# Optimization experiments

Hardware: AMD Instinct MI355X
Metric: run time of the kernel (lower is better)

The kernel has to match this reference:

```python
import jax, jax.numpy as jnp
import numpy as np

B, N = 32, 1024
STEPS = 6

def setup_inputs() -> dict:
    key = jax.random.key(0)
    ks = jax.random.split(key, 20)
    # index columns: residue (<20), element (<5), ordinal position (<21)
    res = jax.random.randint(ks[0], (B, N, 1), 0, 20)
    atom = jax.random.randint(ks[1], (B, N, 1), 0, 5)
    cnt = jax.random.randint(ks[2], (B, N, 1), 0, 21)
    x_int = jnp.concatenate([res, atom, cnt], axis=2)
    x_xyz = jax.random.normal(ks[3], (B, N, 3), dtype=jnp.float32)
    def lin(k, out_d, in_d):
        s = 1.0 / np.sqrt(in_d)
        kw, kb = jax.random.split(k)
        return (jax.random.uniform(kw, (out_d, in_d), jnp.float32, -s, s),
                jax.random.uniform(kb, (out_d,), jnp.float32, -s, s))
    xyz_w, xyz_b = lin(ks[4], 172, 3)
    up_w, up_b = lin(ks[5], 1024, 256)
    att1_w, att1_b = lin(ks[6], 128, 2048)
    att2_w, att2_b = lin(ks[7], 1, 128)
    energy_w, energy_b = lin(ks[8], 1, 1024)
    s = 1.0 / np.sqrt(1024)
    w_ih = jax.random.uniform(ks[9], (4096, 2048), jnp.float32, -s, s)
    w_hh = jax.random.uniform(ks[10], (4096, 1024), jnp.float32, -s, s)
    b_ih = jax.random.uniform(ks[11], (4096,), jnp.float32, -s, s)
    b_hh = jax.random.uniform(ks[12], (4096,), jnp.float32, -s, s)
    amino_embed = jax.random.normal(ks[13], (20, 28), dtype=jnp.float32)
    element_embed = jax.random.normal(ks[14], (5, 28), dtype=jnp.float32)
    position_embed = jax.random.normal(ks[15], (21, 28), dtype=jnp.float32)
    return dict(x_int=x_int, x_xyz=x_xyz,
                amino_embed=amino_embed, element_embed=element_embed,
                position_embed=position_embed, xyz_w=xyz_w, xyz_b=xyz_b,
                up_w=up_w, up_b=up_b, w_ih=w_ih, w_hh=w_hh, b_ih=b_ih, b_hh=b_hh,
                att1_w=att1_w, att1_b=att1_b, att2_w=att2_w, att2_b=att2_b,
                energy_w=energy_w, energy_b=energy_b)

def reference(x_int, x_xyz, amino_embed, element_embed, position_embed,
              xyz_w, xyz_b, up_w, up_b, w_ih, w_hh, b_ih, b_hh,
              att1_w, att1_b, att2_w, att2_b, energy_w, energy_b):
    # embed_atoms: [B,N,28]*3 + [B,N,172] -> [B,N,256]
    emb = jnp.concatenate([
        amino_embed[x_int[:, :, 0]],
        element_embed[x_int[:, :, 1]],
        position_embed[x_int[:, :, 2]],
        jax.nn.relu(jnp.einsum('bnd,od->bno', x_xyz, xyz_w) + xyz_b),
    ], axis=2)
    x = jnp.einsum('bnd,od->bno', emb, up_w) + up_b  # [B,N,1024]
    b = x.shape[0]
    h = jnp.zeros((b, 1024), x.dtype)
    c = jnp.zeros((b, 1024), x.dtype)
    input_embed = jnp.concatenate([x.mean(axis=1), jnp.zeros((b, 1024), x.dtype)], axis=1)
    for _ in range(STEPS):
        # single LSTM cell step (seq_len=1); PyTorch gate order i,f,g,o
        gates = input_embed @ w_ih.T + b_ih + h @ w_hh.T + b_hh
        ig, fg, gg, og = jnp.split(gates, 4, axis=1)
        c = jax.nn.sigmoid(fg) * c + jax.nn.sigmoid(ig) * jnp.tanh(gg)
        h = jax.nn.sigmoid(og) * jnp.tanh(c)
        read = h  # [B,1024]
        # attention MLP over the concat [read | x]: split the 2048-dim GEMM
        a1 = jax.nn.relu(jnp.einsum('bnd,od->bno', x, att1_w[:, 1024:])
                         + (read @ att1_w[:, :1024].T)[:, None, :] + att1_b)
        logits = jnp.einsum('bnk,ok->bno', a1, att2_w) + att2_b  # [B,N,1]
        w = jax.nn.softmax(logits, axis=1)
        pooled = (w * x).sum(axis=1)  # [B,1024]
        input_embed = jnp.concatenate([pooled, read], axis=1)
    return c @ energy_w.T + energy_b  # [B,1]
```

## Files before the change

### kernel.cpp

```cpp
#include <hip/hip_runtime.h>
#include <math.h>

#define BB 32
#define NN 1024
#define BN (BB*NN)
#define KS 24
#define KCH 128

__device__ __forceinline__ float sigmoidf_(float v) { return 1.0f / (1.0f + expf(-v)); }
__device__ __forceinline__ unsigned f2bf(float f) {
  unsigned u = __float_as_uint(f);
  return (u + 0x7fffu + ((u >> 16) & 1u)) >> 16;
}

__global__ void k_zero(float* __restrict__ h, float* __restrict__ c) {
  int i = blockIdx.x * 256 + threadIdx.x;
  h[i] = 0.0f; c[i] = 0.0f;
}

__global__ void k_emb(const int* __restrict__ xint, const float* __restrict__ xyz,
                      const float* __restrict__ am, const float* __restrict__ el,
                      const float* __restrict__ po, const float* __restrict__ xw,
                      const float* __restrict__ xb, float* __restrict__ emb,
                      unsigned* __restrict__ embh) {
  __shared__ float sv[256];
  int row = blockIdx.x;
  int d = threadIdx.x;
  int i0 = xint[row*3+0], i1 = xint[row*3+1], i2 = xint[row*3+2];
  float v;
  if (d < 28)        v = am[i0*28 + d];
  else if (d < 56)   v = el[i1*28 + (d-28)];
  else if (d < 84)   v = po[i2*28 + (d-56)];
  else {
    int o = d - 84;
    float x0 = xyz[row*3+0], x1 = xyz[row*3+1], x2 = xyz[row*3+2];
    v = fmaxf(xw[o*3+0]*x0 + xw[o*3+1]*x1 + xw[o*3+2]*x2 + xb[o], 0.0f);
  }
  emb[(size_t)row*256 + d] = v;
  sv[d] = v;
  __syncthreads();
  if (d < 128) {
    unsigned u = (f2bf(sv[d*2+1]) << 16) | f2bf(sv[d*2]);
    embh[(size_t)row*128 + d] = u;
  }
}

__global__ __launch_bounds__(256) void k_wt(const float* __restrict__ w_ih,
        const float* __restrict__ w_hh, unsigned* __restrict__ wt2) {
  __shared__ float t[32][33];
  int jt = blockIdx.x * 32, kt = blockIdx.y * 32;
  int tx = threadIdx.x & 31, ty = threadIdx.x >> 5;
#pragma unroll
  for (int i = 0; i < 4; i++) {
    int j = jt + ty + i*8;
    int k = kt + tx;
    float v = (k < 2048) ? w_ih[(size_t)j*2048 + k] : w_hh[(size_t)j*1024 + (k - 2048)];
    t[ty + i*8][tx] = v;
  }
  __syncthreads();
#pragma unroll
  for (int i = 0; i < 2; i++) {
    int kl2 = ty + i*8;
    float lo = t[tx][kl2*2], hi = t[tx][kl2*2+1];
    unsigned u = (f2bf(hi) << 16) | f2bf(lo);
    wt2[(size_t)((kt >> 1) + kl2)*4096 + jt + tx] = u;
  }
}

__global__ void k_wc1(const float* __restrict__ up_w, const float* __restrict__ att1w,
                      float* __restrict__ wcp) {
  int k = blockIdx.x;
  int och = blockIdx.y;
  int d = threadIdx.x;
  __shared__ float s[128];
  int o0 = och*128;
  if (d < 128) s[d] = att1w[(size_t)k*2048 + 1024 + o0 + d];
  __syncthreads();
  float acc = 0.0f;
#pragma unroll 8
  for (int oi = 0; oi < 128; oi++) acc += up_w[(size_t)(o0+oi)*256 + d] * s[oi];
  wcp[((size_t)och*128 + k)*256 + d] = acc;
}

__global__ void k_wc2(const float* __restrict__ wcp, float* __restrict__ wc) {
  int k = blockIdx.x, d = threadIdx.x;
  float s = 0.0f;
#pragma unroll
  for (int p = 0; p < 8; p++) s += wcp[((size_t)p*128 + k)*256 + d];
  wc[k*256 + d] = s;
}

__global__ void k_bc(const float* __restrict__ up_b, const float* __restrict__ att1w,
                     float* __restrict__ bc) {
  int k = blockIdx.x;
  int t = threadIdx.x;
  float acc = 0.0f;
#pragma unroll
  for (int i = 0; i < 4; i++) {
    int o = i*256 + t*4;
    float4 a4 = *(const float4*)(att1w + (size_t)k*2048 + 1024 + o);
    float4 b4 = *(const float4*)(up_b + o);
    acc += a4.x*b4.x + a4.y*b4.y + a4.z*b4.z + a4.w*b4.w;
  }
#pragma unroll
  for (int m = 32; m >= 1; m >>= 1) acc += __shfl_xor(acc, m, 64);
  if (t == 0) bc[k] = acc;
}

__global__ __launch_bounds__(256) void k_gemm32(const float* __restrict__ A,
        const float* __restrict__ W, const float* __restrict__ bias,
        float* __restrict__ C) {
  __shared__ float As[32][33];
  __shared__ float Bs[32][132];
  const int m0 = blockIdx.x * 32;
  const int tid = threadIdx.x;
  const int tx = tid & 15, ty = tid >> 4;
  float acc[2][8];
#pragma unroll
  for (int i = 0; i < 2; i++)
#pragma unroll
    for (int j = 0; j < 8; j++) acc[i][j] = 0.0f;

  for (int kt = 0; kt < 256; kt += 32) {
    {
      int r = tid >> 3;
      int kq = (tid & 7) * 4;
      float4 a4 = *(const float4*)(A + (size_t)(m0 + r)*256 + kt + kq);
      As[kq+0][r] = a4.x; As[kq+1][r] = a4.y; As[kq+2][r] = a4.z; As[kq+3][r] = a4.w;
    }
#pragma unroll
    for (int i = 0; i < 4; i++) {
      int s = tid + i*256;
      int n = s >> 3;
      int kq = (s & 7) * 4;
      float4 b4 = *(const float4*)(W + (size_t)n*256 + kt + kq);
      Bs[kq+0][n] = b4.x; Bs[kq+1][n] = b4.y; Bs[kq+2][n] = b4.z; Bs[kq+3][n] = b4.w;
    }
    __syncthreads();
#pragma unroll
    for (int kk = 0; kk < 32; kk++) {
      float a0 = As[kk][ty*2], a1 = As[kk][ty*2+1];
      float4 b0 = *(const float4*)&Bs[kk][tx*4];
      float4 b1 = *(const float4*)&Bs[kk][64 + tx*4];
      float bv[8] = {b0.x,b0.y,b0.z,b0.w,b1.x,b1.y,b1.z,b1.w};
#pragma unroll
      for (int j = 0; j < 8; j++) { acc[0][j] += a0*bv[j]; acc[1][j] += a1*bv[j]; }
    }
    __syncthreads();
  }
#pragma unroll
  for (int i = 0; i < 2; i++) {
    int row = m0 + ty*2 + i;
#pragma unroll
    for (int ch = 0; ch < 2; ch++) {
      int col = ch*64 + tx*4;
      float4 o;
      o.x = acc[i][ch*4+0] + bias[col+0];
      o.y = acc[i][ch*4+1] + bias[col+1];
      o.z = acc[i][ch*4+2] + bias[col+2];
      o.w = acc[i][ch*4+3] + bias[col+3];
      *(float4*)(C + (size_t)row*128 + col) = o;
    }
  }
}

__global__ __launch_bounds__(256) void k_gates(const float* __restrict__ P, const float* __restrict__ h,
        const unsigned* __restrict__ wt2, float* __restrict__ gp) {
  __shared__ float Xs[32][KCH];
  int jb = blockIdx.x;
  int ks = blockIdx.y;
  int tid = threadIdx.x;
  int kglob = ks * KCH;
  const float* src; int soff;
  if (ks < 8)       { src = P; soff = kglob; }
  else if (ks < 16) { src = h; soff = kglob - 1024; }
  else              { src = h; soff = kglob - 2048; }
#pragma unroll
  for (int i = 0; i < 4; i++) {
    int s = tid + i*256;
    int b = s >> 5, k4 = s & 31;
    *(float4*)&Xs[b][k4*4] = *(const float4*)(src + b*1024 + soff + k4*4);
  }
  __syncthreads();

  int jg = tid & 31, bg = tid >> 5;
  int j0 = jb*128 + jg*4;
  int b0 = bg*4;
  const unsigned* wr = wt2 + (size_t)(ks*64)*4096 + j0;
  float acc[4][4];
#pragma unroll
  for (int i = 0; i < 4; i++)
#pragma unroll
    for (int j = 0; j < 4; j++) acc[i][j] = 0.0f;

  for (int k2 = 0; k2 < KCH/2; k2++) {
    uint4 u4 = *(const uint4*)(wr + (size_t)k2*4096);
    float wlo[4], whi[4];
    wlo[0] = __uint_as_float(u4.x << 16); whi[0] = __uint_as_float(u4.x & 0xffff0000u);
    wlo[1] = __uint_as_float(u4.y << 16); whi[1] = __uint_as_float(u4.y & 0xffff0000u);
    wlo[2] = __uint_as_float(u4.z << 16); whi[2] = __uint_as_float(u4.z & 0xffff0000u);
    wlo[3] = __uint_as_float(u4.w << 16); whi[3] = __uint_as_float(u4.w & 0xffff0000u);
    int k = k2*2;
#pragma unroll
    for (int bi = 0; bi < 4; bi++) {
      float x0 = Xs[b0+bi][k], x1 = Xs[b0+bi][k+1];
#pragma unroll
      for (int ji = 0; ji < 4; ji++) acc[ji][bi] += wlo[ji]*x0 + whi[ji]*x1;
    }
  }
#pragma unroll
  for (int bi = 0; bi < 4; bi++) {
    float4 v = make_float4(acc[0][bi], acc[1][bi], acc[2][bi], acc[3][bi]);
    *(float4*)(gp + ((size_t)ks*32 + b0 + bi)*4096 + j0) = v;
  }
}

__global__ __launch_bounds__(256) void k_lstm_rap(const float* __restrict__ gp,
        const float* __restrict__ b_ih, const float* __restrict__ b_hh,
        float* __restrict__ c, float* __restrict__ h,
        const float* __restrict__ att1w, float* __restrict__ rap, int need_ra) {
  int wb = blockIdx.x;
  int b = wb >> 2, dch = wb & 3;
  int tid = threadIdx.x;
  int d = dch*256 + tid;
  __shared__ float hs[256];
  float gi = b_ih[d]        + b_hh[d];
  float gf = b_ih[1024 + d] + b_hh[1024 + d];
  float gg = b_ih[2048 + d] + b_hh[2048 + d];
  float go = b_ih[3072 + d] + b_hh[3072 + d];
#pragma unroll 4
  for (int ks = 0; ks < KS; ks++) {
    const float* base = gp + ((size_t)ks*32 + b)*4096;
    gi += base[d]; gf += base[1024 + d]; gg += base[2048 + d]; go += base[3072 + d];
  }
  size_t ci = (size_t)b*1024 + d;
  float cn = sigmoidf_(gf)*c[ci] + sigmoidf_(gi)*tanhf(gg);
  c[ci] = cn;
  float hn = sigmoidf_(go)*tanhf(cn);
  h[ci] = hn;
  hs[tid] = hn;
  __syncthreads();
  if (need_ra) {
    int k = tid >> 1, half = tid & 1;
    const float* wr = att1w + (size_t)k*2048 + dch*256 + half*128;
    float acc = 0.0f;
#pragma unroll 8
    for (int i = 0; i < 32; i++) {
      float4 w4 = *(const float4*)(wr + i*4);
      int dl = half*128 + i*4;
      acc += w4.x*hs[dl] + w4.y*hs[dl+1] + w4.z*hs[dl+2] + w4.w*hs[dl+3];
    }
    acc += __shfl_xor(acc, 1, 64);
    if (half == 0) rap[((size_t)dch*32 + b)*128 + k] = acc;
  }
}

__global__ __launch_bounds__(256) void k_logits(const float* __restrict__ xa,
        const float* __restrict__ rap, const float* __restrict__ att1b,
        const float* __restrict__ att2w, const float* __restrict__ att2b,
        float* __restrict__ lg) {
  int b = blockIdx.x, nc = blockIdx.y;
  int t = threadIdx.x;
  __shared__ float rb[128], w2[128];
  if (t < 128) {
    float r = rap[(size_t)(0  + b)*128 + t] + rap[(size_t)(32 + b)*128 + t]
            + rap[(size_t)(64 + b)*128 + t] + rap[(size_t)(96 + b)*128 + t];
    rb[t] = r + att1b[t];
    w2[t] = att2w[t];
  }
  __syncthreads();
  int n = nc*128 + (t >> 1);
  int half = (t & 1) * 64;
  const float* xr = xa + ((size_t)b*1024 + n)*128 + half;
  float acc = 0.0f;
#pragma unroll
  for (int i = 0; i < 16; i++) {
    int kk = i*4;
    float4 v = *(const float4*)(xr + kk);
    int kg = half + kk;
    acc += fmaxf(v.x + rb[kg+0], 0.0f)*w2[kg+0]
         + fmaxf(v.y + rb[kg+1], 0.0f)*w2[kg+1]
         + fmaxf(v.z + rb[kg+2], 0.0f)*w2[kg+2]
         + fmaxf(v.w + rb[kg+3], 0.0f)*w2[kg+3];
  }
  acc += __shfl_xor(acc, 1, 64);
  if ((t & 1) == 0) lg[(size_t)b*1024 + n] = acc + att2b[0];
}

__global__ __launch_bounds__(256) void k_poolemb(const unsigned* __restrict__ embh,
        const float* __restrict__ lg, float* __restrict__ pp) {
  int wb = blockIdx.x;
  int b = wb >> 2, nch = wb & 3;
  int tid = threadIdx.x;
  __shared__ float ws[256];
  __shared__ float red[256];
  if (lg) {
    float mx = -1e30f;
#pragma unroll
    for (int i = 0; i < 4; i++) mx = fmaxf(mx, lg[b*1024 + tid + i*256]);
    red[tid] = mx; __syncthreads();
    for (int s = 128; s > 0; s >>= 1) { if (tid < s) red[tid] = fmaxf(red[tid], red[tid+s]); __syncthreads(); }
    float m = red[0]; __syncthreads();
    float sum = 0.0f;
#pragma unroll
    for (int i = 0; i < 4; i++) sum += expf(lg[b*1024 + tid + i*256] - m);
    red[tid] = sum; __syncthreads();
    for (int s = 128; s > 0; s >>= 1) { if (tid < s) red[tid] += red[tid+s]; __syncthreads(); }
    float inv = 1.0f / red[0];
    __syncthreads();
    ws[tid] = expf(lg[b*1024 + nch*256 + tid] - m) * inv;
  } else {
    ws[tid] = 1.0f;
  }
  __syncthreads();
  int pu = tid & 127, ng = tid >> 7;
  const unsigned* eb = embh + (size_t)(b*1024 + nch*256 + ng*128)*128 + pu;
  float a0 = 0.0f, a1 = 0.0f;
#pragma unroll 4
  for (int n = 0; n < 128; n++) {
    unsigned u = eb[(size_t)n*128];
    float w = ws[ng*128 + n];
    a0 += w * __uint_as_float(u << 16);
    a1 += w * __uint_as_float(u & 0xffff0000u);
  }
  int p = nch*2 + ng;
  pp[((size_t)p*32 + b)*256 + pu*2]     = a0;
  pp[((size_t)p*32 + b)*256 + pu*2 + 1] = a1;
}

__global__ __launch_bounds__(256) void k_pool_pgemm(const float* __restrict__ pp,
        const float* __restrict__ up_w, const float* __restrict__ up_b,
        float* __restrict__ Pout, float scale) {
  int wb = blockIdx.x;
  int b = wb >> 2, oc = wb & 3;
  int tid = threadIdx.x;
  __shared__ float pe[256];
  float s = 0.0f;
#pragma unroll
  for (int p = 0; p < 8; p++) s += pp[((size_t)p*32 + b)*256 + tid];
  pe[tid] = s * scale;
  __syncthreads();
  int o = oc*256 + tid;
  const float* wr = up_w + (size_t)o*256;
  float acc = up_b[o];
#pragma unroll 8
  for (int d = 0; d < 256; d += 4) {
    float4 w4 = *(const float4*)(wr + d);
    acc += w4.x*pe[d] + w4.y*pe[d+1] + w4.z*pe[d+2] + w4.w*pe[d+3];
  }
  Pout[(size_t)b*1024 + o] = acc;
}

__global__ void k_out(const float* __restrict__ c, const float* __restrict__ ew,
                      const float* __restrict__ eb, float* __restrict__ out) {
  int b = blockIdx.x, t = threadIdx.x;
  float acc = 0.0f;
  for (int d = t; d < 1024; d += 64) acc += c[b*1024 + d] * ew[d];
  for (int off = 32; off > 0; off >>= 1) acc += __shfl_down(acc, off, 64);
  if (t == 0) out[b] = acc + eb[0];
}

extern "C" void kernel_launch(void* const* d_in, const int* in_sizes, int n_in,
                              void* d_out, int out_size, void* d_ws, size_t ws_size,
                              hipStream_t stream) {
  const int*   x_int  = (const int*)d_in[0];
  const float* x_xyz  = (const float*)d_in[1];
  const float* am     = (const float*)d_in[2];
  const float* el     = (const float*)d_in[3];
  const float* po     = (const float*)d_in[4];
  const float* xyz_w  = (const float*)d_in[5];
  const float* xyz_b  = (const float*)d_in[6];
  const float* up_w   = (const float*)d_in[7];
  const float* up_b   = (const float*)d_in[8];
  const float* w_ih   = (const float*)d_in[9];
  const float* w_hh   = (const float*)d_in[10];
  const float* b_ih   = (const float*)d_in[11];
  const float* b_hh   = (const float*)d_in[12];
  const float* att1_w = (const float*)d_in[13];
  const float* att1_b = (const float*)d_in[14];
  const float* att2_w = (const float*)d_in[15];
  const float* att2_b = (const float*)d_in[16];
  const float* en_w   = (const float*)d_in[17];
  const float* en_b   = (const float*)d_in[18];
  float* out = (float*)d_out;

  char* ws = (char*)d_ws;
  size_t off = 0;
  auto alloc = [&](size_t bytes) { void* p = ws + off; off += (bytes + 255) & ~(size_t)255; return p; };
  float*    emb  = (float*)alloc((size_t)BN*256*4);
  unsigned* embh = (unsigned*)alloc((size_t)BN*128*4);
  unsigned* wt2  = (unsigned*)alloc((size_t)1536*4096*4);
  float*    xa   = (float*)alloc((size_t)BN*128*4);
  float*    wcp  = (float*)alloc((size_t)8*128*256*4);
  float*    wc   = (float*)alloc((size_t)128*256*4);
  float*    bc   = (float*)alloc((size_t)128*4);
  float*    gp   = (float*)alloc((size_t)KS*32*4096*4);
  float*    pp   = (float*)alloc((size_t)8*32*256*4);
  float*    P    = (float*)alloc((size_t)32*1024*4);
  float*    h    = (float*)alloc((size_t)32*1024*4);
  float*    c    = (float*)alloc((size_t)32*1024*4);
  float*    rap  = (float*)alloc((size_t)4*32*128*4);
  float*    lg   = (float*)alloc((size_t)32*1024*4);
  (void)ws_size; (void)in_sizes; (void)n_in; (void)out_size;

  k_zero<<<128, 256, 0, stream>>>(h, c);
  k_emb<<<BN, 256, 0, stream>>>(x_int, x_xyz, am, el, po, xyz_w, xyz_b, emb, embh);
  k_wt<<<dim3(128, 96), 256, 0, stream>>>(w_ih, w_hh, wt2);
  k_wc1<<<dim3(128, 8), 256, 0, stream>>>(up_w, att1_w, wcp);
  k_wc2<<<128, 256, 0, stream>>>(wcp, wc);
  k_bc<<<128, 64, 0, stream>>>(up_b, att1_w, bc);
  k_gemm32<<<BN/32, 256, 0, stream>>>(emb, wc, bc, xa);
  k_poolemb<<<128, 256, 0, stream>>>(embh, nullptr, pp);
  k_pool_pgemm<<<128, 256, 0, stream>>>(pp, up_w, up_b, P, 1.0f/1024.0f);

  for (int step = 0; step < 6; step++) {
    k_gates<<<dim3(32, KS), 256, 0, stream>>>(P, h, wt2, gp);
    k_lstm_rap<<<128, 256, 0, stream>>>(gp, b_ih, b_hh, c, h, att1_w, rap, step < 5 ? 1 : 0);
    if (step < 5) {
      k_logits<<<dim3(32, 8), 256, 0, stream>>>(xa, rap, att1_b, att2_w, att2_b, lg);
      k_poolemb<<<128, 256, 0, stream>>>(embh, lg, pp);
      k_pool_pgemm<<<128, 256, 0, stream>>>(pp, up_w, up_b, P, 1.0f);
    }
  }
  k_out<<<32, 64, 0, stream>>>(c, en_w, en_b, out);
}
```

Baseline: 434.6 us.

## Fuse attention logits into pooling, store projected x in bf16, skip zero-h gates

Merges the logits kernel into the pooling kernel, so each block recomputes the logits for its whole batch row into shared memory instead of reading them from a global buffer. This removes a launch and a round trip through global memory on every step. The precomputed attention projection xa is now stored as bf16, halving the bytes read each step at some cost in precision. The first LSTM step launches only the input-part K-slices, because h starts at zero, so h no longer needs zeroing. The trade-off is redundancy: each of the 4 blocks per batch now recomputes all 1024 logits, which is 4x the logit arithmetic and xa reads.

```diff
diff --git a/kernel.cpp b/kernel.cpp
--- a/kernel.cpp
+++ b/kernel.cpp
@@ -12,10 +12,12 @@
   unsigned u = __float_as_uint(f);
   return (u + 0x7fffu + ((u >> 16) & 1u)) >> 16;
 }
-
-__global__ void k_zero(float* __restrict__ h, float* __restrict__ c) {
+__device__ __forceinline__ float bflo(unsigned u) { return __uint_as_float(u << 16); }
+__device__ __forceinline__ float bfhi(unsigned u) { return __uint_as_float(u & 0xffff0000u); }
+
+__global__ void k_zero(float* __restrict__ c) {
   int i = blockIdx.x * 256 + threadIdx.x;
-  h[i] = 0.0f; c[i] = 0.0f;
+  c[i] = 0.0f;
 }
 
 __global__ void k_emb(const int* __restrict__ xint, const float* __restrict__ xyz,
@@ -109,9 +111,9 @@
 
 __global__ __launch_bounds__(256) void k_gemm32(const float* __restrict__ A,
         const float* __restrict__ W, const float* __restrict__ bias,
-        float* __restrict__ C) {
+        unsigned* __restrict__ Ch) {
   __shared__ float As[32][33];
-  __shared__ float Bs[32][132];
+  __shared__ float Bs[32][133];
   const int m0 = blockIdx.x * 32;
   const int tid = threadIdx.x;
   const int tx = tid & 15, ty = tid >> 4;
@@ -154,12 +156,14 @@
 #pragma unroll
     for (int ch = 0; ch < 2; ch++) {
       int col = ch*64 + tx*4;
-      float4 o;
-      o.x = acc[i][ch*4+0] + bias[col+0];
-      o.y = acc[i][ch*4+1] + bias[col+1];
-      o.z = acc[i][ch*4+2] + bias[col+2];
-      o.w = acc[i][ch*4+3] + bias[col+3];
-      *(float4*)(C + (size_t)row*128 + col) = o;
+      float c0 = acc[i][ch*4+0] + bias[col+0];
+      float c1 = acc[i][ch*4+1] + bias[col+1];
+      float c2 = acc[i][ch*4+2] + bias[col+2];
+      float c3 = acc[i][ch*4+3] + bias[col+3];
+      uint2 o;
+      o.x = (f2bf(c1) << 16) | f2bf(c0);
+      o.y = (f2bf(c3) << 16) | f2bf(c2);
+      *(uint2*)(Ch + (size_t)row*64 + col/2) = o;
     }
   }
 }
@@ -196,10 +200,10 @@
   for (int k2 = 0; k2 < KCH/2; k2++) {
     uint4 u4 = *(const uint4*)(wr + (size_t)k2*4096);
     float wlo[4], whi[4];
-    wlo[0] = __uint_as_float(u4.x << 16); whi[0] = __uint_as_float(u4.x & 0xffff0000u);
-    wlo[1] = __uint_as_float(u4.y << 16); whi[1] = __uint_as_float(u4.y & 0xffff0000u);
-    wlo[2] = __uint_as_float(u4.z << 16); whi[2] = __uint_as_float(u4.z & 0xffff0000u);
-    wlo[3] = __uint_as_float(u4.w << 16); whi[3] = __uint_as_float(u4.w & 0xffff0000u);
+    wlo[0] = bflo(u4.x); whi[0] = bfhi(u4.x);
+    wlo[1] = bflo(u4.y); whi[1] = bfhi(u4.y);
+    wlo[2] = bflo(u4.z); whi[2] = bfhi(u4.z);
+    wlo[3] = bflo(u4.w); whi[3] = bfhi(u4.w);
     int k = k2*2;
 #pragma unroll
     for (int bi = 0; bi < 4; bi++) {
@@ -218,7 +222,8 @@
 __global__ __launch_bounds__(256) void k_lstm_rap(const float* __restrict__ gp,
         const float* __restrict__ b_ih, const float* __restrict__ b_hh,
         float* __restrict__ c, float* __restrict__ h,
-        const float* __restrict__ att1w, float* __restrict__ rap, int need_ra) {
+        const float* __restrict__ att1w, float* __restrict__ rap,
+        int need_ra, int nks) {
   int wb = blockIdx.x;
   int b = wb >> 2, dch = wb & 3;
   int tid = threadIdx.x;
@@ -229,7 +234,7 @@
   float gg = b_ih[2048 + d] + b_hh[2048 + d];
   float go = b_ih[3072 + d] + b_hh[3072 + d];
 #pragma unroll 4
-  for (int ks = 0; ks < KS; ks++) {
+  for (int ks = 0; ks < nks; ks++) {
     const float* base = gp + ((size_t)ks*32 + b)*4096;
     gi += base[d]; gf += base[1024 + d]; gg += base[2048 + d]; go += base[3072 + d];
   }
@@ -255,60 +260,61 @@
   }
 }
 
-__global__ __launch_bounds__(256) void k_logits(const float* __restrict__ xa,
+__global__ __launch_bounds__(256) void k_pool_att(const unsigned* __restrict__ xah,
         const float* __restrict__ rap, const float* __restrict__ att1b,
         const float* __restrict__ att2w, const float* __restrict__ att2b,
-        float* __restrict__ lg) {
-  int b = blockIdx.x, nc = blockIdx.y;
-  int t = threadIdx.x;
-  __shared__ float rb[128], w2[128];
-  if (t < 128) {
-    float r = rap[(size_t)(0  + b)*128 + t] + rap[(size_t)(32 + b)*128 + t]
-            + rap[(size_t)(64 + b)*128 + t] + rap[(size_t)(96 + b)*128 + t];
-    rb[t] = r + att1b[t];
-    w2[t] = att2w[t];
-  }
-  __syncthreads();
-  int n = nc*128 + (t >> 1);
-  int half = (t & 1) * 64;
-  const float* xr = xa + ((size_t)b*1024 + n)*128 + half;
-  float acc = 0.0f;
-#pragma unroll
-  for (int i = 0; i < 16; i++) {
-    int kk = i*4;
-    float4 v = *(const float4*)(xr + kk);
-    int kg = half + kk;
-    acc += fmaxf(v.x + rb[kg+0], 0.0f)*w2[kg+0]
-         + fmaxf(v.y + rb[kg+1], 0.0f)*w2[kg+1]
-         + fmaxf(v.z + rb[kg+2], 0.0f)*w2[kg+2]
-         + fmaxf(v.w + rb[kg+3], 0.0f)*w2[kg+3];
-  }
-  acc += __shfl_xor(acc, 1, 64);
-  if ((t & 1) == 0) lg[(size_t)b*1024 + n] = acc + att2b[0];
-}
-
-__global__ __launch_bounds__(256) void k_poolemb(const unsigned* __restrict__ embh,
-        const float* __restrict__ lg, float* __restrict__ pp) {
+        const unsigned* __restrict__ embh, float* __restrict__ pp) {
   int wb = blockIdx.x;
   int b = wb >> 2, nch = wb & 3;
   int tid = threadIdx.x;
+  __shared__ float rb[128], w2[128];
+  __shared__ float lgs[1024];
+  __shared__ float red[256];
   __shared__ float ws[256];
-  __shared__ float red[256];
-  if (lg) {
+  if (xah) {
+    if (tid < 128) {
+      float r = rap[(size_t)(0  + b)*128 + tid] + rap[(size_t)(32 + b)*128 + tid]
+              + rap[(size_t)(64 + b)*128 + tid] + rap[(size_t)(96 + b)*128 + tid];
+      rb[tid] = r + att1b[tid];
+      w2[tid] = att2w[tid];
+    }
+    __syncthreads();
+    float a2b = att2b[0];
+#pragma unroll
+    for (int i = 0; i < 4; i++) {
+      int n = tid + i*256;
+      const uint4* xr = (const uint4*)(xah + ((size_t)b*1024 + n)*64);
+      float acc = a2b;
+#pragma unroll 4
+      for (int q = 0; q < 16; q++) {
+        uint4 u4 = xr[q];
+        int k = q*8;
+        acc += fmaxf(bflo(u4.x) + rb[k+0], 0.0f)*w2[k+0]
+             + fmaxf(bfhi(u4.x) + rb[k+1], 0.0f)*w2[k+1]
+             + fmaxf(bflo(u4.y) + rb[k+2], 0.0f)*w2[k+2]
+             + fmaxf(bfhi(u4.y) + rb[k+3], 0.0f)*w2[k+3]
+             + fmaxf(bflo(u4.z) + rb[k+4], 0.0f)*w2[k+4]
+             + fmaxf(bfhi(u4.z) + rb[k+5], 0.0f)*w2[k+5]
+             + fmaxf(bflo(u4.w) + rb[k+6], 0.0f)*w2[k+6]
+             + fmaxf(bfhi(u4.w) + rb[k+7], 0.0f)*w2[k+7];
+      }
+      lgs[n] = acc;
+    }
+    __syncthreads();
     float mx = -1e30f;
 #pragma unroll
-    for (int i = 0; i < 4; i++) mx = fmaxf(mx, lg[b*1024 + tid + i*256]);
+    for (int i = 0; i < 4; i++) mx = fmaxf(mx, lgs[tid + i*256]);
     red[tid] = mx; __syncthreads();
     for (int s = 128; s > 0; s >>= 1) { if (tid < s) red[tid] = fmaxf(red[tid], red[tid+s]); __syncthreads(); }
     float m = red[0]; __syncthreads();
     float sum = 0.0f;
 #pragma unroll
-    for (int i = 0; i < 4; i++) sum += expf(lg[b*1024 + tid + i*256] - m);
+    for (int i = 0; i < 4; i++) sum += expf(lgs[tid + i*256] - m);
     red[tid] = sum; __syncthreads();
     for (int s = 128; s > 0; s >>= 1) { if (tid < s) red[tid] += red[tid+s]; __syncthreads(); }
     float inv = 1.0f / red[0];
     __syncthreads();
-    ws[tid] = expf(lg[b*1024 + nch*256 + tid] - m) * inv;
+    ws[tid] = expf(lgs[nch*256 + tid] - m) * inv;
   } else {
     ws[tid] = 1.0f;
   }
@@ -320,8 +326,8 @@
   for (int n = 0; n < 128; n++) {
     unsigned u = eb[(size_t)n*128];
     float w = ws[ng*128 + n];
-    a0 += w * __uint_as_float(u << 16);
-    a1 += w * __uint_as_float(u & 0xffff0000u);
+    a0 += w * bflo(u);
+    a1 += w * bfhi(u);
   }
   int p = nch*2 + ng;
   pp[((size_t)p*32 + b)*256 + pu*2]     = a0;
@@ -390,7 +396,7 @@
   float*    emb  = (float*)alloc((size_t)BN*256*4);
   unsigned* embh = (unsigned*)alloc((size_t)BN*128*4);
   unsigned* wt2  = (unsigned*)alloc((size_t)1536*4096*4);
-  float*    xa   = (float*)alloc((size_t)BN*128*4);
+  unsigned* xah  = (unsigned*)alloc((size_t)BN*64*4);
   float*    wcp  = (float*)alloc((size_t)8*128*256*4);
   float*    wc   = (float*)alloc((size_t)128*256*4);
   float*    bc   = (float*)alloc((size_t)128*4);
@@ -400,25 +406,25 @@
   float*    h    = (float*)alloc((size_t)32*1024*4);
   float*    c    = (float*)alloc((size_t)32*1024*4);
   float*    rap  = (float*)alloc((size_t)4*32*128*4);
-  float*    lg   = (float*)alloc((size_t)32*1024*4);
   (void)ws_size; (void)in_sizes; (void)n_in; (void)out_size;
 
-  k_zero<<<128, 256, 0, stream>>>(h, c);
+  k_zero<<<128, 256, 0, stream>>>(c);
   k_emb<<<BN, 256, 0, stream>>>(x_int, x_xyz, am, el, po, xyz_w, xyz_b, emb, embh);
   k_wt<<<dim3(128, 96), 256, 0, stream>>>(w_ih, w_hh, wt2);
   k_wc1<<<dim3(128, 8), 256, 0, stream>>>(up_w, att1_w, wcp);
   k_wc2<<<128, 256, 0, stream>>>(wcp, wc);
   k_bc<<<128, 64, 0, stream>>>(up_b, att1_w, bc);
-  k_gemm32<<<BN/32, 256, 0, stream>>>(emb, wc, bc, xa);
-  k_poolemb<<<128, 256, 0, stream>>>(embh, nullptr, pp);
+  k_gemm32<<<BN/32, 256, 0, stream>>>(emb, wc, bc, xah);
+  k_pool_att<<<128, 256, 0, stream>>>(nullptr, rap, att1_b, att2_w, att2_b, embh, pp);
   k_pool_pgemm<<<128, 256, 0, stream>>>(pp, up_w, up_b, P, 1.0f/1024.0f);
 
   for (int step = 0; step < 6; step++) {
-    k_gates<<<dim3(32, KS), 256, 0, stream>>>(P, h, wt2, gp);
-    k_lstm_rap<<<128, 256, 0, stream>>>(gp, b_ih, b_hh, c, h, att1_w, rap, step < 5 ? 1 : 0);
+    int nks = (step == 0) ? 8 : KS;
+    k_gates<<<dim3(32, nks), 256, 0, stream>>>(P, h, wt2, gp);
+    k_lstm_rap<<<128, 256, 0, stream>>>(gp, b_ih, b_hh, c, h, att1_w, rap,
+                                        step < 5 ? 1 : 0, nks);
     if (step < 5) {
-      k_logits<<<dim3(32, 8), 256, 0, stream>>>(xa, rap, att1_b, att2_w, att2_b, lg);
-      k_poolemb<<<128, 256, 0, stream>>>(embh, lg, pp);
+      k_pool_att<<<128, 256, 0, stream>>>(xah, rap, att1_b, att2_w, att2_b, embh, pp);
       k_pool_pgemm<<<128, 256, 0, stream>>>(pp, up_w, up_b, P, 1.0f);
     }
   }
```

After: 480.6 us, median of 2. +10.6%, slower.

## Use split-bf16 MFMA for attention projection GEMM and skip zero-state gate work

Applied to the files above, without the earlier changes.

Replaces the fp32 SIMT GEMM that computes the projected attention features with a bf16 MFMA kernel. It keeps accuracy by splitting each operand into a high and a low bf16 part and using three MFMA products. The fp32 embedding buffer is dropped in favour of packed hi/lo bf16 buffers, which cuts the write traffic in the embedding kernel. On the first LSTM step the gate GEMM runs only over the 8 K-slices fed by the pooled input, skipping the h and zero-input slices, so zeroing h is no longer needed. The cost is three MFMAs per tile, and B fragments are read straight from global memory without LDS staging.

```diff
diff --git a/kernel.cpp b/kernel.cpp
--- a/kernel.cpp
+++ b/kernel.cpp
@@ -7,22 +7,27 @@
 #define KS 24
 #define KCH 128
 
+using bf16x8 = __attribute__((ext_vector_type(8))) short;
+using f32x4  = __attribute__((ext_vector_type(4))) float;
+
 __device__ __forceinline__ float sigmoidf_(float v) { return 1.0f / (1.0f + expf(-v)); }
 __device__ __forceinline__ unsigned f2bf(float f) {
   unsigned u = __float_as_uint(f);
   return (u + 0x7fffu + ((u >> 16) & 1u)) >> 16;
 }
-
-__global__ void k_zero(float* __restrict__ h, float* __restrict__ c) {
+__device__ __forceinline__ float bflo(unsigned u) { return __uint_as_float(u << 16); }
+__device__ __forceinline__ float bfhi(unsigned u) { return __uint_as_float(u & 0xffff0000u); }
+
+__global__ void k_zero(float* __restrict__ c) {
   int i = blockIdx.x * 256 + threadIdx.x;
-  h[i] = 0.0f; c[i] = 0.0f;
+  c[i] = 0.0f;
 }
 
 __global__ void k_emb(const int* __restrict__ xint, const float* __restrict__ xyz,
                       const float* __restrict__ am, const float* __restrict__ el,
                       const float* __restrict__ po, const float* __restrict__ xw,
-                      const float* __restrict__ xb, float* __restrict__ emb,
-                      unsigned* __restrict__ embh) {
+                      const float* __restrict__ xb,
+                      unsigned* __restrict__ embh, unsigned* __restrict__ embl) {
   __shared__ float sv[256];
   int row = blockIdx.x;
   int d = threadIdx.x;
@@ -36,12 +41,15 @@
     float x0 = xyz[row*3+0], x1 = xyz[row*3+1], x2 = xyz[row*3+2];
     v = fmaxf(xw[o*3+0]*x0 + xw[o*3+1]*x1 + xw[o*3+2]*x2 + xb[o], 0.0f);
   }
-  emb[(size_t)row*256 + d] = v;
   sv[d] = v;
   __syncthreads();
   if (d < 128) {
-    unsigned u = (f2bf(sv[d*2+1]) << 16) | f2bf(sv[d*2]);
-    embh[(size_t)row*128 + d] = u;
+    float v0 = sv[d*2], v1 = sv[d*2+1];
+    unsigned h0 = f2bf(v0), h1 = f2bf(v1);
+    embh[(size_t)row*128 + d] = (h1 << 16) | h0;
+    float l0 = v0 - __uint_as_float(h0 << 16);
+    float l1 = v1 - __uint_as_float(h1 << 16);
+    embl[(size_t)row*128 + d] = (f2bf(l1) << 16) | f2bf(l0);
   }
 }
 
@@ -82,12 +90,23 @@
   wcp[((size_t)och*128 + k)*256 + d] = acc;
 }
 
-__global__ void k_wc2(const float* __restrict__ wcp, float* __restrict__ wc) {
-  int k = blockIdx.x, d = threadIdx.x;
+__global__ void k_wc2(const float* __restrict__ wcp, unsigned* __restrict__ wchh,
+                      unsigned* __restrict__ wchl) {
+  __shared__ float sv[256];
+  int n = blockIdx.x, d = threadIdx.x;
   float s = 0.0f;
 #pragma unroll
-  for (int p = 0; p < 8; p++) s += wcp[((size_t)p*128 + k)*256 + d];
-  wc[k*256 + d] = s;
+  for (int p = 0; p < 8; p++) s += wcp[((size_t)p*128 + n)*256 + d];
+  sv[d] = s;
+  __syncthreads();
+  if (d < 128) {
+    float v0 = sv[d*2], v1 = sv[d*2+1];
+    unsigned h0 = f2bf(v0), h1 = f2bf(v1);
+    wchh[n*128 + d] = (h1 << 16) | h0;
+    float l0 = v0 - __uint_as_float(h0 << 16);
+    float l1 = v1 - __uint_as_float(h1 << 16);
+    wchl[n*128 + d] = (f2bf(l1) << 16) | f2bf(l0);
+  }
 }
 
 __global__ void k_bc(const float* __restrict__ up_b, const float* __restrict__ att1w,
@@ -107,60 +126,50 @@
   if (t == 0) bc[k] = acc;
 }
 
-__global__ __launch_bounds__(256) void k_gemm32(const float* __restrict__ A,
-        const float* __restrict__ W, const float* __restrict__ bias,
-        float* __restrict__ C) {
-  __shared__ float As[32][33];
-  __shared__ float Bs[32][132];
-  const int m0 = blockIdx.x * 32;
-  const int tid = threadIdx.x;
-  const int tx = tid & 15, ty = tid >> 4;
-  float acc[2][8];
-#pragma unroll
-  for (int i = 0; i < 2; i++)
-#pragma unroll
-    for (int j = 0; j < 8; j++) acc[i][j] = 0.0f;
-
-  for (int kt = 0; kt < 256; kt += 32) {
-    {
-      int r = tid >> 3;
-      int kq = (tid & 7) * 4;
-      float4 a4 = *(const float4*)(A + (size_t)(m0 + r)*256 + kt + kq);
-      As[kq+0][r] = a4.x; As[kq+1][r] = a4.y; As[kq+2][r] = a4.z; As[kq+3][r] = a4.w;
+__global__ __launch_bounds__(256) void k_gemm_mfma(
+    const unsigned* __restrict__ Ahp, const unsigned* __restrict__ Alp,
+    const unsigned* __restrict__ Bhp, const unsigned* __restrict__ Blp,
+    const float* __restrict__ bias, float* __restrict__ C) {
+  const short* Ah = (const short*)Ahp;
+  const short* Al = (const short*)Alp;
+  const short* Bh = (const short*)Bhp;
+  const short* Bl = (const short*)Blp;
+  int tid = threadIdx.x;
+  int wid = tid >> 6, l = tid & 63;
+  int m0 = blockIdx.x*32 + (wid >> 1)*16;
+  int n0 = (wid & 1)*64;
+  int kb = (l >> 4)*8;
+  int row = m0 + (l & 15);
+  f32x4 acc0 = {0,0,0,0}, acc1 = {0,0,0,0}, acc2 = {0,0,0,0}, acc3 = {0,0,0,0};
+  const short* arh = Ah + (size_t)row*256 + kb;
+  const short* arl = Al + (size_t)row*256 + kb;
+  int ncol = n0 + (l & 15);
+  const short* brh = Bh + (size_t)ncol*256 + kb;
+  const short* brl = Bl + (size_t)ncol*256 + kb;
+#pragma unroll
+  for (int k0 = 0; k0 < 256; k0 += 32) {
+    bf16x8 ah = *(const bf16x8*)(arh + k0);
+    bf16x8 al = *(const bf16x8*)(arl + k0);
+#pragma unroll
+    for (int nt = 0; nt < 4; nt++) {
+      bf16x8 bh = *(const bf16x8*)(brh + (size_t)nt*16*256 + k0);
+      bf16x8 bl = *(const bf16x8*)(brl + (size_t)nt*16*256 + k0);
+      f32x4 a = (nt == 0) ? acc0 : (nt == 1) ? acc1 : (nt == 2) ? acc2 : acc3;
+      a = __builtin_amdgcn_mfma_f32_16x16x32_bf16(ah, bh, a, 0, 0, 0);
+      a = __builtin_amdgcn_mfma_f32_16x16x32_bf16(al, bh, a, 0, 0, 0);
+      a = __builtin_amdgcn_mfma_f32_16x16x32_bf16(ah, bl, a, 0, 0, 0);
+      if (nt == 0) acc0 = a; else if (nt == 1) acc1 = a; else if (nt == 2) acc2 = a; else acc3 = a;
     }
-#pragma unroll
-    for (int i = 0; i < 4; i++) {
-      int s = tid + i*256;
-      int n = s >> 3;
-      int kq = (s & 7) * 4;
-      float4 b4 = *(const float4*)(W + (size_t)n*256 + kt + kq);
-      Bs[kq+0][n] = b4.x; Bs[kq+1][n] = b4.y; Bs[kq+2][n] = b4.z; Bs[kq+3][n] = b4.w;
-    }
-    __syncthreads();
-#pragma unroll
-    for (int kk = 0; kk < 32; kk++) {
-      float a0 = As[kk][ty*2], a1 = As[kk][ty*2+1];
-      float4 b0 = *(const float4*)&Bs[kk][tx*4];
-      float4 b1 = *(const float4*)&Bs[kk][64 + tx*4];
-      float bv[8] = {b0.x,b0.y,b0.z,b0.w,b1.x,b1.y,b1.z,b1.w};
-#pragma unroll
-      for (int j = 0; j < 8; j++) { acc[0][j] += a0*bv[j]; acc[1][j] += a1*bv[j]; }
-    }
-    __syncthreads();
-  }
-#pragma unroll
-  for (int i = 0; i < 2; i++) {
-    int row = m0 + ty*2 + i;
-#pragma unroll
-    for (int ch = 0; ch < 2; ch++) {
-      int col = ch*64 + tx*4;
-      float4 o;
-      o.x = acc[i][ch*4+0] + bias[col+0];
-      o.y = acc[i][ch*4+1] + bias[col+1];
-      o.z = acc[i][ch*4+2] + bias[col+2];
-      o.w = acc[i][ch*4+3] + bias[col+3];
-      *(float4*)(C + (size_t)row*128 + col) = o;
-    }
+  }
+  int r0 = m0 + (l >> 4)*4;
+#pragma unroll
+  for (int nt = 0; nt < 4; nt++) {
+    f32x4 a = (nt == 0) ? acc0 : (nt == 1) ? acc1 : (nt == 2) ? acc2 : acc3;
+    int col = n0 + nt*16 + (l & 15);
+    float bv = bias[col];
+#pragma unroll
+    for (int i = 0; i < 4; i++)
+      C[(size_t)(r0 + i)*128 + col] = a[i] + bv;
   }
 }
 
@@ -196,10 +205,10 @@
   for (int k2 = 0; k2 < KCH/2; k2++) {
     uint4 u4 = *(const uint4*)(wr + (size_t)k2*4096);
     float wlo[4], whi[4];
-    wlo[0] = __uint_as_float(u4.x << 16); whi[0] = __uint_as_float(u4.x & 0xffff0000u);
-    wlo[1] = __uint_as_float(u4.y << 16); whi[1] = __uint_as_float(u4.y & 0xffff0000u);
-    wlo[2] = __uint_as_float(u4.z << 16); whi[2] = __uint_as_float(u4.z & 0xffff0000u);
-    wlo[3] = __uint_as_float(u4.w << 16); whi[3] = __uint_as_float(u4.w & 0xffff0000u);
+    wlo[0] = bflo(u4.x); whi[0] = bfhi(u4.x);
+    wlo[1] = bflo(u4.y); whi[1] = bfhi(u4.y);
+    wlo[2] = bflo(u4.z); whi[2] = bfhi(u4.z);
+    wlo[3] = bflo(u4.w); whi[3] = bfhi(u4.w);
     int k = k2*2;
 #pragma unroll
     for (int bi = 0; bi < 4; bi++) {
@@ -218,7 +227,8 @@
 __global__ __launch_bounds__(256) void k_lstm_rap(const float* __restrict__ gp,
         const float* __restrict__ b_ih, const float* __restrict__ b_hh,
         float* __restrict__ c, float* __restrict__ h,
-        const float* __restrict__ att1w, float* __restrict__ rap, int need_ra) {
+        const float* __restrict__ att1w, float* __restrict__ rap,
+        int need_ra, int nks) {
   int wb = blockIdx.x;
   int b = wb >> 2, dch = wb & 3;
   int tid = threadIdx.x;
@@ -229,7 +239,7 @@
   float gg = b_ih[2048 + d] + b_hh[2048 + d];
   float go = b_ih[3072 + d] + b_hh[3072 + d];
 #pragma unroll 4
-  for (int ks = 0; ks < KS; ks++) {
+  for (int ks = 0; ks < nks; ks++) {
     const float* base = gp + ((size_t)ks*32 + b)*4096;
     gi += base[d]; gf += base[1024 + d]; gg += base[2048 + d]; go += base[3072 + d];
   }
@@ -320,8 +330,8 @@
   for (int n = 0; n < 128; n++) {
     unsigned u = eb[(size_t)n*128];
     float w = ws[ng*128 + n];
-    a0 += w * __uint_as_float(u << 16);
-    a1 += w * __uint_as_float(u & 0xffff0000u);
+    a0 += w * bflo(u);
+    a1 += w * bfhi(u);
   }
   int p = nch*2 + ng;
   pp[((size_t)p*32 + b)*256 + pu*2]     = a0;
@@ -387,12 +397,13 @@
   char* ws = (char*)d_ws;
   size_t off = 0;
   auto alloc = [&](size_t bytes) { void* p = ws + off; off += (bytes + 255) & ~(size_t)255; return p; };
-  float*    emb  = (float*)alloc((size_t)BN*256*4);
   unsigned* embh = (unsigned*)alloc((size_t)BN*128*4);
+  unsigned* embl = (unsigned*)alloc((size_t)BN*128*4);
   unsigned* wt2  = (unsigned*)alloc((size_t)1536*4096*4);
   float*    xa   = (float*)alloc((size_t)BN*128*4);
   float*    wcp  = (float*)alloc((size_t)8*128*256*4);
-  float*    wc   = (float*)alloc((size_t)128*256*4);
+  unsigned* wchh = (unsigned*)alloc((size_t)128*128*4);
+  unsigned* wchl = (unsigned*)alloc((size_t)128*128*4);
   float*    bc   = (float*)alloc((size_t)128*4);
   float*    gp   = (float*)alloc((size_t)KS*32*4096*4);
   float*    pp   = (float*)alloc((size_t)8*32*256*4);
@@ -403,19 +414,21 @@
   float*    lg   = (float*)alloc((size_t)32*1024*4);
   (void)ws_size; (void)in_sizes; (void)n_in; (void)out_size;
 
-  k_zero<<<128, 256, 0, stream>>>(h, c);
-  k_emb<<<BN, 256, 0, stream>>>(x_int, x_xyz, am, el, po, xyz_w, xyz_b, emb, embh);
+  k_zero<<<128, 256, 0, stream>>>(c);
+  k_emb<<<BN, 256, 0, stream>>>(x_int, x_xyz, am, el, po, xyz_w, xyz_b, embh, embl);
   k_wt<<<dim3(128, 96), 256, 0, stream>>>(w_ih, w_hh, wt2);
   k_wc1<<<dim3(128, 8), 256, 0, stream>>>(up_w, att1_w, wcp);
-  k_wc2<<<128, 256, 0, stream>>>(wcp, wc);
+  k_wc2<<<128, 256, 0, stream>>>(wcp, wchh, wchl);
   k_bc<<<128, 64, 0, stream>>>(up_b, att1_w, bc);
-  k_gemm32<<<BN/32, 256, 0, stream>>>(emb, wc, bc, xa);
+  k_gemm_mfma<<<BN/32, 256, 0, stream>>>(embh, embl, wchh, wchl, bc, xa);
   k_poolemb<<<128, 256, 0, stream>>>(embh, nullptr, pp);
   k_pool_pgemm<<<128, 256, 0, stream>>>(pp, up_w, up_b, P, 1.0f/1024.0f);
 
   for (int step = 0; step < 6; step++) {
-    k_gates<<<dim3(32, KS), 256, 0, stream>>>(P, h, wt2, gp);
-    k_lstm_rap<<<128, 256, 0, stream>>>(gp, b_ih, b_hh, c, h, att1_w, rap, step < 5 ? 1 : 0);
+    int nks = (step == 0) ? 8 : KS;
+    k_gates<<<dim3(32, nks), 256, 0, stream>>>(P, h, wt2, gp);
+    k_lstm_rap<<<128, 256, 0, stream>>>(gp, b_ih, b_hh, c, h, att1_w, rap,
+                                        step < 5 ? 1 : 0, nks);
     if (step < 5) {
       k_logits<<<dim3(32, 8), 256, 0, stream>>>(xa, rap, att1_b, att2_w, att2_b, lg);
       k_poolemb<<<128, 256, 0, stream>>>(embh, lg, pp);
```

After: 429.9 us. No clear change (-1.1%).
